# Kernel optimization log

Measured on AMD Instinct MI355X. Metric: run time of the kernel, lower is better.

## Reference

```python
import jax, jax.numpy as jnp
import numpy as np

N = 50000          # nodes
E = 500000         # edges (avg degree 10)
WIDTH = 128        # node feature width
HID = 128          # width * scale, scale=1 -> 2 heads of 64
HEAD = 64          # head_dim (module-level constant)
EMB = WIDTH // 2   # edge-embed width = 64
RES = 1.0
BOND = (5, 6, 2, 17)  # bond_size vocabularies


def setup_inputs() -> dict:
    key = jax.random.key(0)
    ks = jax.random.split(key, 24)
    w = lambda k, s: (jax.random.normal(k, s, jnp.float32) * 0.02)
    inp = {
        "x": jax.random.normal(ks[0], (N, WIDTH), jnp.float32),
        "edge_index": jax.random.randint(ks[1], (2, E), 0, N),
        "edge_attr": jax.random.randint(ks[2], (E, 4), 0, 3),
        # pre: Linear(width, width)
        "pre_w": w(ks[3], (WIDTH, WIDTH)), "pre_b": jnp.zeros((WIDTH,), jnp.float32),
        # msg[0..3]: Linear(width, hidden)
        "msg0_w": w(ks[4], (WIDTH, HID)), "msg0_b": jnp.zeros((HID,), jnp.float32),
        "msg1_w": w(ks[5], (WIDTH, HID)), "msg1_b": jnp.zeros((HID,), jnp.float32),
        "msg2_w": w(ks[6], (WIDTH, HID)), "msg2_b": jnp.zeros((HID,), jnp.float32),
        "msg3_w": w(ks[7], (WIDTH, HID)), "msg3_b": jnp.zeros((HID,), jnp.float32),
        # remix[0..2]: Linear(width//2, hidden)
        "remix0_w": w(ks[8], (EMB, HID)), "remix0_b": jnp.zeros((HID,), jnp.float32),
        "remix1_w": w(ks[9], (EMB, HID)), "remix1_b": jnp.zeros((HID,), jnp.float32),
        "remix2_w": w(ks[10], (EMB, HID)), "remix2_b": jnp.zeros((HID,), jnp.float32),
        # post: Linear(hidden, width)
        "post_w": w(ks[11], (HID, WIDTH)), "post_b": jnp.zeros((WIDTH,), jnp.float32),
        # EmbedBlock tables (bond_size + 1 rows each); tables 1..3 have padding_idx=0
        "emb0": w(ks[12], (BOND[0] + 1, EMB)),
        "emb1": w(ks[13], (BOND[1] + 1, EMB)).at[0].set(0.0),
        "emb2": w(ks[14], (BOND[2] + 1, EMB)).at[0].set(0.0),
        "emb3": w(ks[15], (BOND[3] + 1, EMB)).at[0].set(0.0),
        "einit": jnp.zeros((4,), jnp.float32),          # EmbedBlock.init0
        "init0": jnp.zeros((4,), jnp.float32),          # ConvBlock.init0 (hop*2+2)
    }
    return inp


def _gelu(v):
    return jax.nn.gelu(v, approximate=False)


def _ln(v):
    m = jnp.mean(v, axis=-1, keepdims=True)
    var = jnp.mean(jnp.square(v - m), axis=-1, keepdims=True)
    return (v - m) / jnp.sqrt(var + 1e-5)


def reference(x, edge_index, edge_attr, pre_w, pre_b, msg0_w, msg0_b,
              msg1_w, msg1_b, msg2_w, msg2_b, msg3_w, msg3_b,
              remix0_w, remix0_b, remix1_w, remix1_b, remix2_w, remix2_b,
              post_w, post_b, emb0, emb1, emb2, emb3, einit, init0):
    n = x.shape[0]
    e = edge_index.shape[1]
    xx = _ln(x @ pre_w + pre_b)  # pre: Linear + LayerNorm(no affine)
    # EmbedBlock: weighted sum of per-column embeddings, xw = exp(a)/sqrt(sum exp(a))
    xw = jnp.exp(einit) / jnp.sqrt(jnp.sum(jnp.exp(einit)))
    ee = (emb0[edge_attr[:, 0]] * xw[0] + emb1[edge_attr[:, 1]] * xw[1]
          + emb2[edge_attr[:, 2]] * xw[2] + emb3[edge_attr[:, 3]] * xw[3])  # [E, 64]
    src, dst = edge_index[0], edge_index[1]  # source_to_target: j=src, i=dst
    x_j = xx[src]
    x_i = xx[dst]
    scale_e = jnp.exp(init0[-2])
    scale_v = jnp.exp(init0[-1])
    q = x_i @ msg1_w + msg1_b + (ee @ remix0_w + remix0_b) * scale_e  # [E, HID]
    k = x_j @ msg2_w + msg2_b + (ee @ remix1_w + remix1_b) * scale_e
    v = _gelu(x_j @ msg3_w + msg3_b + (ee @ remix2_w + remix2_b) * scale_v)
    # per-head attention score, head_dim = 64
    att = jnp.sum((q * k).reshape(e, -1, HEAD), axis=-1, keepdims=True) / np.sqrt(HEAD)
    att = jnp.exp(att * init0[0] + init0[1])  # edge_type=0, hop=1
    msg = (v.reshape(e, -1, HEAD) * att).reshape(e, -1)  # [E, HID]
    agg = jax.ops.segment_sum(msg, dst, num_segments=n)  # scatter-add to targets
    xx = _gelu(xx @ msg0_w + msg0_b) + agg
    out = xx @ post_w + post_b
    return x + out * RES
```

## Files before the change

### kernel.cpp

```cpp
#include <hip/hip_runtime.h>
#include <cstdint>

#define WIDTH 128
#define NCOMBO 2268
#define XSL 136
#define OSL 132

typedef short bf16x8 __attribute__((ext_vector_type(8)));
typedef float f32x4  __attribute__((ext_vector_type(4)));

__device__ __forceinline__ float gelu_fast(float v) {
    float e = __expf(v * __builtin_fmaf(v * v, 0.0713548f, 1.5957691f));
    return v - v * __builtin_amdgcn_rcpf(e + 1.0f);
}
__device__ __forceinline__ short f2b(float f) {
    unsigned u = __float_as_uint(f);
    unsigned r = (u + 0x7FFFu + ((u >> 16) & 1u)) >> 16;
    return (short)r;
}
__device__ __forceinline__ float b2f_lo(unsigned u) { return __uint_as_float(u << 16); }
__device__ __forceinline__ float b2f_hi(unsigned u) { return __uint_as_float(u & 0xFFFF0000u); }
__device__ __forceinline__ unsigned pack2(float lo, float hi) {
    return (unsigned)(unsigned short)f2b(lo) | ((unsigned)(unsigned short)f2b(hi) << 16);
}

__global__ void k_prep(const float* __restrict__ einit, const float* __restrict__ init0,
                       const float* __restrict__ emb0, const float* __restrict__ emb1,
                       const float* __restrict__ emb2, const float* __restrict__ emb3,
                       const float* __restrict__ r0w, const float* __restrict__ r0b,
                       const float* __restrict__ r1w, const float* __restrict__ r1b,
                       const float* __restrict__ r2w, const float* __restrict__ r2b,
                       const float* __restrict__ pw0, const float* __restrict__ pw1,
                       const float* __restrict__ pw2, const float* __restrict__ pw3,
                       const float* __restrict__ pw4, const float* __restrict__ pw5,
                       short* __restrict__ o0, short* __restrict__ o1,
                       short* __restrict__ o2, short* __restrict__ o3,
                       short* __restrict__ o4, short* __restrict__ o5,
                       float* __restrict__ U, float* __restrict__ scal,
                       int* __restrict__ counts, int n) {
    int tid = blockIdx.x * blockDim.x + threadIdx.x;
    if (tid == 0) { scal[0] = init0[0]; scal[1] = init0[1]; }
    const int TOTW = 6 * 16384;
    const int TOTU = 3 * 34 * WIDTH;
    if (tid < TOTW) {
        int which = tid >> 14;
        int r = tid & 16383;
        int t    = r >> 11;
        int kc   = (r >> 9) & 3;
        int lane = (r >> 3) & 63;
        int j    = r & 7;
        int k  = kc * 32 + ((lane >> 4) << 3) + j;
        int nn = (t << 4) + (lane & 15);
        const float* w = (which == 0) ? pw0 : (which == 1) ? pw1 : (which == 2) ? pw2
                       : (which == 3) ? pw3 : (which == 4) ? pw4 : pw5;
        short* o = (which == 0) ? o0 : (which == 1) ? o1 : (which == 2) ? o2
                 : (which == 3) ? o3 : (which == 4) ? o4 : o5;
        o[r] = f2b(w[k * 128 + nn]);
    } else if (tid < TOTW + TOTU) {
        int idx = tid - TOTW;
        float e0 = expf(einit[0]), e1 = expf(einit[1]), e2 = expf(einit[2]), e3 = expf(einit[3]);
        float inv = 1.0f / sqrtf(e0 + e1 + e2 + e3);
        float xw[4] = {e0 * inv, e1 * inv, e2 * inv, e3 * inv};
        float se = expf(init0[2]);
        float sv = expf(init0[3]);
        int r   = idx / (34 * WIDTH);
        int rem = idx - r * (34 * WIDTH);
        int g   = rem / WIDTH;
        int j   = rem - g * WIDTH;
        int cc, base;
        if (g >= 16)      { cc = 3; base = 16; }
        else if (g >= 13) { cc = 2; base = 13; }
        else if (g >= 6)  { cc = 1; base = 6; }
        else              { cc = 0; base = 0; }
        int i = g - base;
        const float* em = (cc == 0) ? emb0 : (cc == 1) ? emb1 : (cc == 2) ? emb2 : emb3;
        const float* w  = (r == 0) ? r0w : (r == 1) ? r1w : r2w;
        const float* rb = (r == 0) ? r0b : (r == 1) ? r1b : r2b;
        float s = (r == 2) ? sv : se;
        float acc = 0.0f;
        const float* erow = em + i * 64;
        for (int d = 0; d < 64; ++d) acc += erow[d] * w[d * WIDTH + j];
        float val = s * xw[cc] * acc;
        if (cc == 0) val += s * rb[j];
        U[idx] = val;
    } else if (tid < TOTW + TOTU + n) {
        counts[tid - TOTW - TOTU] = 0;
    }
}

__global__ void k_prepc(const float* __restrict__ U, const float* __restrict__ init0,
                        float* __restrict__ Uc) {
    int bi = blockIdx.x;
    int r  = bi / NCOMBO;
    if (r < 2 && init0[0] == 0.0f) return;
    int cb = bi - r * NCOMBO;
    int a  = cb / 378;
    int rm = cb - a * 378;
    int b  = rm / 54;
    rm -= b * 54;
    int c  = rm / 18;
    int d  = rm - c * 18;
    int j  = threadIdx.x;
    const float* Ur = U + r * 34 * WIDTH;
    Uc[(size_t)bi * WIDTH + j] = Ur[a * WIDTH + j] + Ur[(6 + b) * WIDTH + j]
                               + Ur[(13 + c) * WIDTH + j] + Ur[(16 + d) * WIDTH + j];
}

__global__ void k_hist(const int* __restrict__ edge_index, int* __restrict__ counts,
                       int* __restrict__ rank, int E) {
    int e = blockIdx.x * blockDim.x + threadIdx.x;
    if (e >= E) return;
    rank[e] = atomicAdd(&counts[edge_index[E + e]], 1);
}

__global__ void k_scan1(const int* __restrict__ counts, int* __restrict__ lscan,
                        int* __restrict__ partials, int n) {
    __shared__ int s[256];
    int t = threadIdx.x;
    int i = blockIdx.x * 256 + t;
    int v = (i < n) ? counts[i] : 0;
    s[t] = v;
    __syncthreads();
    for (int d = 1; d < 256; d <<= 1) {
        int u = (t >= d) ? s[t - d] : 0;
        __syncthreads();
        s[t] += u;
        __syncthreads();
    }
    if (i < n) lscan[i] = s[t];
    if (t == 255) partials[blockIdx.x] = s[255];
}

__global__ void k_scan2(int* __restrict__ partials, int nb,
                        int* __restrict__ offsets, int n) {
    __shared__ int s[1024];
    int t = threadIdx.x;
    int v = (t < nb) ? partials[t] : 0;
    s[t] = v;
    __syncthreads();
    for (int d = 1; d < 1024; d <<= 1) {
        int u = (t >= d) ? s[t - d] : 0;
        __syncthreads();
        s[t] += u;
        __syncthreads();
    }
    if (t < nb) partials[t] = s[t] - v;
    if (t == 1023) offsets[n] = s[1023];
}

__global__ void k_scan3(const int* __restrict__ counts, const int* __restrict__ lscan,
                        const int* __restrict__ partials, int* __restrict__ offsets, int n) {
    int i = blockIdx.x * 256 + threadIdx.x;
    if (i >= n) return;
    offsets[i] = partials[blockIdx.x] + lscan[i] - counts[i];
}

__global__ void k_scatter(const int* __restrict__ edge_index, const int* __restrict__ edge_attr,
                          const int* __restrict__ offsets, const int* __restrict__ rank,
                          unsigned* __restrict__ s_pk, int E) {
    int e = blockIdx.x * blockDim.x + threadIdx.x;
    if (e >= E) return;
    int src = edge_index[e];
    int dst = edge_index[E + e];
    int4 at = ((const int4*)edge_attr)[e];
    int combo = ((at.x * 7 + at.y) * 3 + at.z) * 18 + at.w;
    s_pk[offsets[dst] + rank[e]] = (unsigned)src | ((unsigned)combo << 17);
}

__global__ void __launch_bounds__(256, 2) k_gemm12(
        const float* __restrict__ x,
        const short* __restrict__ preF, const float* __restrict__ pre_b,
        const short* __restrict__ w0F, const float* __restrict__ b0,
        const short* __restrict__ w1F, const float* __restrict__ b1,
        const short* __restrict__ w2F, const float* __restrict__ b2,
        const short* __restrict__ w3F, const float* __restrict__ b3,
        const float* __restrict__ scal,
        short* __restrict__ Gb, float* __restrict__ A,
        short* __restrict__ Bb, short* __restrict__ Cb, int n) {
    __shared__ short xs_raw[64 * XSL];
    __shared__ short xs_xx[64 * XSL];
    int tid  = threadIdx.x;
    int w    = tid >> 6;
    int lane = tid & 63;
    int quad = lane >> 4, l16 = lane & 15;
    int m0   = blockIdx.x * 64;

    bf16x8 Bg[2][4], Bc[2][4];
#pragma unroll
    for (int tt = 0; tt < 2; ++tt)
#pragma unroll
        for (int kc = 0; kc < 4; ++kc) {
            int fo = (((2 * w + tt) * 4 + kc) * 64 + lane) * 8;
            Bg[tt][kc] = *(const bf16x8*)(w0F + fo);
            Bc[tt][kc] = *(const bf16x8*)(w3F + fo);
        }

#pragma unroll
    for (int it = 0; it < 8; ++it) {
        int fi  = it * 256 + tid;
        int row = fi >> 5, c4 = fi & 31;
        int gr  = min(m0 + row, n - 1);
        float4 v = ((const float4*)x)[(size_t)gr * 32 + c4];
        uint2 p;
        p.x = pack2(v.x, v.y);
        p.y = pack2(v.z, v.w);
        *(uint2*)(&xs_raw[row * XSL + c4 * 4]) = p;
    }
    __syncthreads();

    {
        bf16x8 a[4];
#pragma unroll
        for (int kc = 0; kc < 4; ++kc)
            a[kc] = *(const bf16x8*)(&xs_raw[(w * 16 + l16) * XSL + kc * 32 + quad * 8]);
        f32x4 acc[8];
#pragma unroll
        for (int t = 0; t < 8; ++t) acc[t] = (f32x4){0.f, 0.f, 0.f, 0.f};
#pragma unroll
        for (int kc = 0; kc < 4; ++kc)
#pragma unroll
            for (int t = 0; t < 8; ++t) {
                bf16x8 b = *(const bf16x8*)(preF + ((t * 4 + kc) * 64 + lane) * 8);
                acc[t] = __builtin_amdgcn_mfma_f32_16x16x32_bf16(a[kc], b, acc[t], 0, 0, 0);
            }
#pragma unroll
        for (int t = 0; t < 8; ++t) {
            float bv = pre_b[t * 16 + l16];
#pragma unroll
            for (int r = 0; r < 4; ++r) acc[t][r] += bv;
        }
#pragma unroll
        for (int r = 0; r < 4; ++r) {
            float s = 0.f, s2 = 0.f;
#pragma unroll
            for (int t = 0; t < 8; ++t) { float v = acc[t][r]; s += v; s2 += v * v; }
            s  += __shfl_xor(s, 1);  s2 += __shfl_xor(s2, 1);
            s  += __shfl_xor(s, 2);  s2 += __shfl_xor(s2, 2);
            s  += __shfl_xor(s, 4);  s2 += __shfl_xor(s2, 4);
            s  += __shfl_xor(s, 8);  s2 += __shfl_xor(s2, 8);
            float m   = s * (1.0f / WIDTH);
            float var = s2 * (1.0f / WIDTH) - m * m;
            float rs  = rsqrtf(var + 1e-5f);
#pragma unroll
            for (int t = 0; t < 8; ++t) acc[t][r] = (acc[t][r] - m) * rs;
        }
        int rowb = w * 16 + quad * 4;
#pragma unroll
        for (int t = 0; t < 8; ++t)
#pragma unroll
            for (int r = 0; r < 4; ++r)
                xs_xx[(rowb + r) * XSL + t * 16 + l16] = f2b(acc[t][r]);
    }
    __syncthreads();

    bf16x8 a2[4][4];
#pragma unroll
    for (int i = 0; i < 4; ++i)
#pragma unroll
        for (int kc = 0; kc < 4; ++kc)
            a2[i][kc] = *(const bf16x8*)(&xs_xx[(i * 16 + l16) * XSL + kc * 32 + quad * 8]);
    __syncthreads();

    {
        f32x4 accG[4][2], accC[4][2];
#pragma unroll
        for (int i = 0; i < 4; ++i)
#pragma unroll
            for (int tt = 0; tt < 2; ++tt) {
                accG[i][tt] = (f32x4){0.f,0.f,0.f,0.f};
                accC[i][tt] = (f32x4){0.f,0.f,0.f,0.f};
            }
#pragma unroll
        for (int kc = 0; kc < 4; ++kc)
#pragma unroll
            for (int i = 0; i < 4; ++i)
#pragma unroll
                for (int tt = 0; tt < 2; ++tt) {
                    accG[i][tt] = __builtin_amdgcn_mfma_f32_16x16x32_bf16(a2[i][kc], Bg[tt][kc], accG[i][tt], 0, 0, 0);
                    accC[i][tt] = __builtin_amdgcn_mfma_f32_16x16x32_bf16(a2[i][kc], Bc[tt][kc], accC[i][tt], 0, 0, 0);
                }
#pragma unroll
        for (int tt = 0; tt < 2; ++tt) {
            int col = (2 * w + tt) * 16 + l16;
            float bg = b0[col];
            float bc = b3[col];
#pragma unroll
            for (int i = 0; i < 4; ++i)
#pragma unroll
                for (int r = 0; r < 4; ++r) {
                    int row = i * 16 + quad * 4 + r;
                    xs_raw[row * XSL + col] = f2b(gelu_fast(accG[i][tt][r] + bg));
                    xs_xx[row * XSL + col]  = f2b(accC[i][tt][r] + bc);
                }
        }
    }
    __syncthreads();

#pragma unroll
    for (int it = 0; it < 4; ++it) {
        int si  = it * 256 + tid;
        int row = si >> 4, c8 = si & 15;
        if (m0 + row < n) {
            *(bf16x8*)(Gb + (size_t)(m0 + row) * WIDTH + c8 * 8) = *(const bf16x8*)(&xs_raw[row * XSL + c8 * 8]);
            *(bf16x8*)(Cb + (size_t)(m0 + row) * WIDTH + c8 * 8) = *(const bf16x8*)(&xs_xx[row * XSL + c8 * 8]);
        }
    }

    if (scal[0] != 0.0f) {
        bf16x8 Ba[2][4], Bbf[2][4];
#pragma unroll
        for (int tt = 0; tt < 2; ++tt)
#pragma unroll
            for (int kc = 0; kc < 4; ++kc) {
                int fo = (((2 * w + tt) * 4 + kc) * 64 + lane) * 8;
                Ba[tt][kc]  = *(const bf16x8*)(w1F + fo);
                Bbf[tt][kc] = *(const bf16x8*)(w2F + fo);
            }
        f32x4 accA[4][2], accB[4][2];
#pragma unroll
        for (int i = 0; i < 4; ++i)
#pragma unroll
            for (int tt = 0; tt < 2; ++tt) {
                accA[i][tt] = (f32x4){0.f,0.f,0.f,0.f};
                accB[i][tt] = (f32x4){0.f,0.f,0.f,0.f};
            }
#pragma unroll
        for (int kc = 0; kc < 4; ++kc)
#pragma unroll
            for (int i = 0; i < 4; ++i)
#pragma unroll
                for (int tt = 0; tt < 2; ++tt) {
                    accA[i][tt] = __builtin_amdgcn_mfma_f32_16x16x32_bf16(a2[i][kc], Ba[tt][kc],  accA[i][tt], 0, 0, 0);
                    accB[i][tt] = __builtin_amdgcn_mfma_f32_16x16x32_bf16(a2[i][kc], Bbf[tt][kc], accB[i][tt], 0, 0, 0);
                }
#pragma unroll
        for (int tt = 0; tt < 2; ++tt) {
            int col = (2 * w + tt) * 16 + l16;
            float ba = b1[col];
            float bb = b2[col];
#pragma unroll
            for (int i = 0; i < 4; ++i)
#pragma unroll
                for (int r = 0; r < 4; ++r) {
                    int row = m0 + i * 16 + quad * 4 + r;
                    if (row < n) {
                        size_t idx = (size_t)row * WIDTH + col;
                        A[idx]  = accA[i][tt][r] + ba;
                        Bb[idx] = f2b(accB[i][tt][r] + bb);
                    }
                }
        }
    }
}

__global__ void __launch_bounds__(256)
k_agg(const int* __restrict__ offsets, const unsigned* __restrict__ s_pk,
      const float* __restrict__ A, const short* __restrict__ Bb,
      const short* __restrict__ Cb, const float* __restrict__ Uc,
      const float* __restrict__ scal, const short* __restrict__ Gb,
      short* __restrict__ hb, int n) {
    int wid = threadIdx.x >> 6;
    int L   = threadIdx.x & 63;
    int node = blockIdx.x * 4 + wid;
    if (node >= n) return;
    int start = offsets[node];
    int end   = offsets[node + 1];

    const unsigned* Cb32 = (const unsigned*)Cb;
    const unsigned* Bb32 = (const unsigned*)Bb;
    const float2* U0c2 = (const float2*)(Uc);
    const float2* U1c2 = (const float2*)(Uc + (size_t)NCOMBO * WIDTH);
    const float2* U2c2 = (const float2*)(Uc + 2 * (size_t)NCOMBO * WIDTH);

    float i0 = scal[0], i1 = scal[1];
    float acc0 = 0.0f, acc1 = 0.0f;

    if (i0 == 0.0f) {
        int p = start;
        for (; p + 4 <= end; p += 4) {
            unsigned pk0 = s_pk[p],     pk1 = s_pk[p + 1];
            unsigned pk2 = s_pk[p + 2], pk3 = s_pk[p + 3];
            unsigned cc0 = Cb32[(pk0 & 0x1FFFFu) * 64 + L];
            unsigned cc1 = Cb32[(pk1 & 0x1FFFFu) * 64 + L];
            unsigned cc2 = Cb32[(pk2 & 0x1FFFFu) * 64 + L];
            unsigned cc3 = Cb32[(pk3 & 0x1FFFFu) * 64 + L];
            float2   uu0 = U2c2[(pk0 >> 17) * 64 + L];
            float2   uu1 = U2c2[(pk1 >> 17) * 64 + L];
            float2   uu2 = U2c2[(pk2 >> 17) * 64 + L];
            float2   uu3 = U2c2[(pk3 >> 17) * 64 + L];
            acc0 += gelu_fast(b2f_lo(cc0) + uu0.x);
            acc1 += gelu_fast(b2f_hi(cc0) + uu0.y);
            acc0 += gelu_fast(b2f_lo(cc1) + uu1.x);
            acc1 += gelu_fast(b2f_hi(cc1) + uu1.y);
            acc0 += gelu_fast(b2f_lo(cc2) + uu2.x);
            acc1 += gelu_fast(b2f_hi(cc2) + uu2.y);
            acc0 += gelu_fast(b2f_lo(cc3) + uu3.x);
            acc1 += gelu_fast(b2f_hi(cc3) + uu3.y);
        }
        if (p + 2 <= end) {
            unsigned pk0 = s_pk[p], pk1 = s_pk[p + 1];
            unsigned cc0 = Cb32[(pk0 & 0x1FFFFu) * 64 + L];
            unsigned cc1 = Cb32[(pk1 & 0x1FFFFu) * 64 + L];
            float2   uu0 = U2c2[(pk0 >> 17) * 64 + L];
            float2   uu1 = U2c2[(pk1 >> 17) * 64 + L];
            acc0 += gelu_fast(b2f_lo(cc0) + uu0.x);
            acc1 += gelu_fast(b2f_hi(cc0) + uu0.y);
            acc0 += gelu_fast(b2f_lo(cc1) + uu1.x);
            acc1 += gelu_fast(b2f_hi(cc1) + uu1.y);
            p += 2;
        }
        if (p < end) {
            unsigned pk0 = s_pk[p];
            unsigned cc0 = Cb32[(pk0 & 0x1FFFFu) * 64 + L];
            float2   uu0 = U2c2[(pk0 >> 17) * 64 + L];
            acc0 += gelu_fast(b2f_lo(cc0) + uu0.x);
            acc1 += gelu_fast(b2f_hi(cc0) + uu0.y);
        }
        float s = __expf(i1);
        acc0 *= s; acc1 *= s;
    } else {
        float2 av = *(const float2*)(A + (size_t)node * WIDTH + 2 * L);
        int p = start;
        for (; p + 2 <= end; p += 2) {
            unsigned pk0 = s_pk[p], pk1 = s_pk[p + 1];
            unsigned sA = pk0 & 0x1FFFFu, cA = pk0 >> 17;
            unsigned sB = pk1 & 0x1FFFFu, cB = pk1 >> 17;
            float2 u0a = U0c2[cA * 64 + L], u0b = U0c2[cB * 64 + L];
            float2 u1a = U1c2[cA * 64 + L], u1b = U1c2[cB * 64 + L];
            float2 u2a = U2c2[cA * 64 + L], u2b = U2c2[cB * 64 + L];
            unsigned bba = Bb32[sA * 64 + L], bbb = Bb32[sB * 64 + L];
            unsigned cca = Cb32[sA * 64 + L], ccb = Cb32[sB * 64 + L];
            {
                float q0 = av.x + u0a.x, q1 = av.y + u0a.y;
                float k0 = b2f_lo(bba) + u1a.x, k1 = b2f_hi(bba) + u1a.y;
                float v0 = gelu_fast(b2f_lo(cca) + u2a.x);
                float v1 = gelu_fast(b2f_hi(cca) + u2a.y);
                float s = q0 * k0 + q1 * k1;
                s += __shfl_xor(s, 1);
                s += __shfl_xor(s, 2);
                s += __shfl_xor(s, 4);
                s += __shfl_xor(s, 8);
                s += __shfl_xor(s, 16);
                float att = __expf(s * 0.125f * i0 + i1);
                acc0 += v0 * att;
                acc1 += v1 * att;
            }
            {
                float q0 = av.x + u0b.x, q1 = av.y + u0b.y;
                float k0 = b2f_lo(bbb) + u1b.x, k1 = b2f_hi(bbb) + u1b.y;
                float v0 = gelu_fast(b2f_lo(ccb) + u2b.x);
                float v1 = gelu_fast(b2f_hi(ccb) + u2b.y);
                float s = q0 * k0 + q1 * k1;
                s += __shfl_xor(s, 1);
                s += __shfl_xor(s, 2);
                s += __shfl_xor(s, 4);
                s += __shfl_xor(s, 8);
                s += __shfl_xor(s, 16);
                float att = __expf(s * 0.125f * i0 + i1);
                acc0 += v0 * att;
                acc1 += v1 * att;
            }
        }
        if (p < end) {
            unsigned pk = s_pk[p];
            unsigned sA = pk & 0x1FFFFu, cA = pk >> 17;
            float2 u0 = U0c2[cA * 64 + L];
            float2 u1 = U1c2[cA * 64 + L];
            float2 u2 = U2c2[cA * 64 + L];
            unsigned bb = Bb32[sA * 64 + L];
            unsigned cc = Cb32[sA * 64 + L];
            float q0 = av.x + u0.x, q1 = av.y + u0.y;
            float k0 = b2f_lo(bb) + u1.x, k1 = b2f_hi(bb) + u1.y;
            float v0 = gelu_fast(b2f_lo(cc) + u2.x);
            float v1 = gelu_fast(b2f_hi(cc) + u2.y);
            float s = q0 * k0 + q1 * k1;
            s += __shfl_xor(s, 1);
            s += __shfl_xor(s, 2);
            s += __shfl_xor(s, 4);
            s += __shfl_xor(s, 8);
            s += __shfl_xor(s, 16);
            float att = __expf(s * 0.125f * i0 + i1);
            acc0 += v0 * att;
            acc1 += v1 * att;
        }
    }
    unsigned g = ((const unsigned*)Gb)[(size_t)node * 64 + L];
    ((unsigned*)hb)[(size_t)node * 64 + L] = pack2(b2f_lo(g) + acc0, b2f_hi(g) + acc1);
}

__global__ void __launch_bounds__(256, 2) k_post(
        const float* __restrict__ x, const short* __restrict__ hb,
        const short* __restrict__ postF, const float* __restrict__ post_b,
        float* __restrict__ out, int n) {
    __shared__ short hs[64 * XSL];
    __shared__ float os[64 * OSL];
    int tid  = threadIdx.x;
    int w    = tid >> 6;
    int lane = tid & 63;
    int quad = lane >> 4, l16 = lane & 15;
    int m0   = blockIdx.x * 64;

    bf16x8 Bp[2][4];
#pragma unroll
    for (int tt = 0; tt < 2; ++tt)
#pragma unroll
        for (int kc = 0; kc < 4; ++kc)
            Bp[tt][kc] = *(const bf16x8*)(postF + (((2 * w + tt) * 4 + kc) * 64 + lane) * 8);

#pragma unroll
    for (int it = 0; it < 4; ++it) {
        int si  = it * 256 + tid;
        int row = si >> 4, c8 = si & 15;
        int gr  = min(m0 + row, n - 1);
        *(bf16x8*)(&hs[row * XSL + c8 * 8]) = *(const bf16x8*)(hb + (size_t)gr * WIDTH + c8 * 8);
    }
    __syncthreads();

    bf16x8 a[4][4];
#pragma unroll
    for (int i = 0; i < 4; ++i)
#pragma unroll
        for (int kc = 0; kc < 4; ++kc)
            a[i][kc] = *(const bf16x8*)(&hs[(i * 16 + l16) * XSL + kc * 32 + quad * 8]);

    f32x4 acc[4][2];
#pragma unroll
    for (int i = 0; i < 4; ++i)
#pragma unroll
        for (int tt = 0; tt < 2; ++tt) acc[i][tt] = (f32x4){0.f,0.f,0.f,0.f};
#pragma unroll
    for (int kc = 0; kc < 4; ++kc)
#pragma unroll
        for (int i = 0; i < 4; ++i)
#pragma unroll
            for (int tt = 0; tt < 2; ++tt)
                acc[i][tt] = __builtin_amdgcn_mfma_f32_16x16x32_bf16(a[i][kc], Bp[tt][kc], acc[i][tt], 0, 0, 0);

#pragma unroll
    for (int tt = 0; tt < 2; ++tt) {
        int col = (2 * w + tt) * 16 + l16;
        float bv = post_b[col];
#pragma unroll
        for (int i = 0; i < 4; ++i)
#pragma unroll
            for (int r = 0; r < 4; ++r)
                os[(i * 16 + quad * 4 + r) * OSL + col] = acc[i][tt][r] + bv;
    }
    __syncthreads();

#pragma unroll
    for (int it = 0; it < 8; ++it) {
        int fi  = it * 256 + tid;
        int row = fi >> 5, c4 = fi & 31;
        if (m0 + row < n) {
            float4 xv = ((const float4*)x)[(size_t)(m0 + row) * 32 + c4];
            float4 av = *(const float4*)(&os[row * OSL + c4 * 4]);
            float4 ov = {xv.x + av.x, xv.y + av.y, xv.z + av.z, xv.w + av.w};
            ((float4*)out)[(size_t)(m0 + row) * 32 + c4] = ov;
        }
    }
}

extern "C" void kernel_launch(void* const* d_in, const int* in_sizes, int n_in,
                              void* d_out, int out_size, void* d_ws, size_t ws_size,
                              hipStream_t stream) {
    const float* x      = (const float*)d_in[0];
    const int*   eidx   = (const int*)d_in[1];
    const int*   eattr  = (const int*)d_in[2];
    const float* pre_w  = (const float*)d_in[3];
    const float* pre_b  = (const float*)d_in[4];
    const float* msg0_w = (const float*)d_in[5];
    const float* msg0_b = (const float*)d_in[6];
    const float* msg1_w = (const float*)d_in[7];
    const float* msg1_b = (const float*)d_in[8];
    const float* msg2_w = (const float*)d_in[9];
    const float* msg2_b = (const float*)d_in[10];
    const float* msg3_w = (const float*)d_in[11];
    const float* msg3_b = (const float*)d_in[12];
    const float* r0w    = (const float*)d_in[13];
    const float* r0b    = (const float*)d_in[14];
    const float* r1w    = (const float*)d_in[15];
    const float* r1b    = (const float*)d_in[16];
    const float* r2w    = (const float*)d_in[17];
    const float* r2b    = (const float*)d_in[18];
    const float* post_w = (const float*)d_in[19];
    const float* post_b = (const float*)d_in[20];
    const float* emb0   = (const float*)d_in[21];
    const float* emb1   = (const float*)d_in[22];
    const float* emb2   = (const float*)d_in[23];
    const float* emb3   = (const float*)d_in[24];
    const float* einit  = (const float*)d_in[25];
    const float* init0  = (const float*)d_in[26];

    int n = in_sizes[0] / WIDTH;
    int E = in_sizes[2] / 4;
    size_t NW = (size_t)n * WIDTH;

    float* ws   = (float*)d_ws;
    float* A    = ws;
    float* U    = ws + NW;
    float* Uc   = U + 3 * 34 * WIDTH;
    float* scal = Uc + 3 * (size_t)NCOMBO * WIDTH;
    short* sw   = (short*)(scal + 2);
    short* preF  = sw;
    short* w0F   = sw + 16384;
    short* w1F   = sw + 2 * 16384;
    short* w2F   = sw + 3 * 16384;
    short* w3F   = sw + 4 * 16384;
    short* postF = sw + 5 * 16384;
    short* Bb    = sw + 6 * 16384;
    short* Cb    = Bb + NW;
    short* Gb    = Cb + NW;
    short* hb    = Gb + NW;
    int*      ib       = (int*)(hb + NW);
    int*      offsets  = ib;
    int*      counts   = offsets + (n + 1);
    int*      lscan    = counts + n;
    int*      partials = lscan + n;
    int*      rank     = partials + 1024;
    unsigned* s_pk     = (unsigned*)(rank + E);

    int prep_total = 6 * 16384 + 3 * 34 * WIDTH + n;
    k_prep<<<(prep_total + 255) / 256, 256, 0, stream>>>(
        einit, init0, emb0, emb1, emb2, emb3,
        r0w, r0b, r1w, r1b, r2w, r2b,
        pre_w, msg0_w, msg1_w, msg2_w, msg3_w, post_w,
        preF, w0F, w1F, w2F, w3F, postF, U, scal, counts, n);
    k_prepc<<<3 * NCOMBO, 128, 0, stream>>>(U, init0, Uc);

    int eb = (E + 255) / 256;
    k_hist<<<eb, 256, 0, stream>>>(eidx, counts, rank, E);
    int sb = (n + 255) / 256;
    k_scan1<<<sb, 256, 0, stream>>>(counts, lscan, partials, n);
    k_scan2<<<1, 1024, 0, stream>>>(partials, sb, offsets, n);
    k_scan3<<<sb, 256, 0, stream>>>(counts, lscan, partials, offsets, n);
    k_scatter<<<eb, 256, 0, stream>>>(eidx, eattr, offsets, rank, s_pk, E);

    int gb = (n + 63) / 64;
    k_gemm12<<<gb, 256, 0, stream>>>(x, preF, pre_b, w0F, msg0_b, w1F, msg1_b,
                                     w2F, msg2_b, w3F, msg3_b, scal, Gb, A, Bb, Cb, n);
    k_agg<<<(n + 3) / 4, 256, 0, stream>>>(offsets, s_pk, A, Bb, Cb, Uc, scal, Gb, hb, n);
    k_post<<<gb, 256, 0, stream>>>(x, hb, postF, post_b, (float*)d_out, n);
}
```

Before: 240.7 us.

## Merge prep, histogram, scan and scatter stages into fewer fused launches

Cuts the launch chain from ten kernels to six. Weight conversion now shares a kernel with the edge histogram, the block scan shares one with the combo-table build, and the offset computation and CSR scatter ride as extra blocks inside the GEMM kernel. The scatter computes offsets inline from partials, lscan and counts instead of waiting on a separate scan3 pass, and counts are zeroed with a memset. This removes several launch gaps and serialisation points, but adds divergent block roles, and GEMM blocks with large LDS use may now share the GPU with light scatter blocks.

```diff
diff --git a/kernel.cpp b/kernel.cpp
--- a/kernel.cpp
+++ b/kernel.cpp
@@ -5,6 +5,8 @@
 #define NCOMBO 2268
 #define XSL 136
 #define OSL 132
+#define TOTW (6 * 16384)
+#define TOTU (3 * 34 * WIDTH)
 
 typedef short bf16x8 __attribute__((ext_vector_type(8)));
 typedef float f32x4  __attribute__((ext_vector_type(4)));
@@ -24,24 +26,23 @@
     return (unsigned)(unsigned short)f2b(lo) | ((unsigned)(unsigned short)f2b(hi) << 16);
 }
 
-__global__ void k_prep(const float* __restrict__ einit, const float* __restrict__ init0,
-                       const float* __restrict__ emb0, const float* __restrict__ emb1,
-                       const float* __restrict__ emb2, const float* __restrict__ emb3,
-                       const float* __restrict__ r0w, const float* __restrict__ r0b,
-                       const float* __restrict__ r1w, const float* __restrict__ r1b,
-                       const float* __restrict__ r2w, const float* __restrict__ r2b,
-                       const float* __restrict__ pw0, const float* __restrict__ pw1,
-                       const float* __restrict__ pw2, const float* __restrict__ pw3,
-                       const float* __restrict__ pw4, const float* __restrict__ pw5,
-                       short* __restrict__ o0, short* __restrict__ o1,
-                       short* __restrict__ o2, short* __restrict__ o3,
-                       short* __restrict__ o4, short* __restrict__ o5,
-                       float* __restrict__ U, float* __restrict__ scal,
-                       int* __restrict__ counts, int n) {
+__global__ void k_f1(const float* __restrict__ einit, const float* __restrict__ init0,
+                     const float* __restrict__ emb0, const float* __restrict__ emb1,
+                     const float* __restrict__ emb2, const float* __restrict__ emb3,
+                     const float* __restrict__ r0w, const float* __restrict__ r0b,
+                     const float* __restrict__ r1w, const float* __restrict__ r1b,
+                     const float* __restrict__ r2w, const float* __restrict__ r2b,
+                     const float* __restrict__ pw0, const float* __restrict__ pw1,
+                     const float* __restrict__ pw2, const float* __restrict__ pw3,
+                     const float* __restrict__ pw4, const float* __restrict__ pw5,
+                     short* __restrict__ o0, short* __restrict__ o1,
+                     short* __restrict__ o2, short* __restrict__ o3,
+                     short* __restrict__ o4, short* __restrict__ o5,
+                     float* __restrict__ U, float* __restrict__ scal,
+                     const int* __restrict__ edge_index, int* __restrict__ counts,
+                     int* __restrict__ rank, int E) {
     int tid = blockIdx.x * blockDim.x + threadIdx.x;
     if (tid == 0) { scal[0] = init0[0]; scal[1] = init0[1]; }
-    const int TOTW = 6 * 16384;
-    const int TOTU = 3 * 34 * WIDTH;
     if (tid < TOTW) {
         int which = tid >> 14;
         int r = tid & 16383;
@@ -83,52 +84,48 @@
         float val = s * xw[cc] * acc;
         if (cc == 0) val += s * rb[j];
         U[idx] = val;
-    } else if (tid < TOTW + TOTU + n) {
-        counts[tid - TOTW - TOTU] = 0;
-    }
-}
-
-__global__ void k_prepc(const float* __restrict__ U, const float* __restrict__ init0,
-                        float* __restrict__ Uc) {
-    int bi = blockIdx.x;
-    int r  = bi / NCOMBO;
-    if (r < 2 && init0[0] == 0.0f) return;
-    int cb = bi - r * NCOMBO;
-    int a  = cb / 378;
-    int rm = cb - a * 378;
-    int b  = rm / 54;
-    rm -= b * 54;
-    int c  = rm / 18;
-    int d  = rm - c * 18;
-    int j  = threadIdx.x;
-    const float* Ur = U + r * 34 * WIDTH;
-    Uc[(size_t)bi * WIDTH + j] = Ur[a * WIDTH + j] + Ur[(6 + b) * WIDTH + j]
-                               + Ur[(13 + c) * WIDTH + j] + Ur[(16 + d) * WIDTH + j];
-}
-
-__global__ void k_hist(const int* __restrict__ edge_index, int* __restrict__ counts,
-                       int* __restrict__ rank, int E) {
-    int e = blockIdx.x * blockDim.x + threadIdx.x;
-    if (e >= E) return;
-    rank[e] = atomicAdd(&counts[edge_index[E + e]], 1);
-}
-
-__global__ void k_scan1(const int* __restrict__ counts, int* __restrict__ lscan,
-                        int* __restrict__ partials, int n) {
-    __shared__ int s[256];
-    int t = threadIdx.x;
-    int i = blockIdx.x * 256 + t;
-    int v = (i < n) ? counts[i] : 0;
-    s[t] = v;
-    __syncthreads();
-    for (int d = 1; d < 256; d <<= 1) {
-        int u = (t >= d) ? s[t - d] : 0;
+    } else if (tid < TOTW + TOTU + E) {
+        int e = tid - TOTW - TOTU;
+        rank[e] = atomicAdd(&counts[edge_index[E + e]], 1);
+    }
+}
+
+__global__ void k_f2(const int* __restrict__ counts, int* __restrict__ lscan,
+                     int* __restrict__ partials, int n, int sb,
+                     const float* __restrict__ U, const float* __restrict__ init0,
+                     float* __restrict__ Uc) {
+    if ((int)blockIdx.x < sb) {
+        __shared__ int s[256];
+        int t = threadIdx.x;
+        int i = blockIdx.x * 256 + t;
+        int v = (i < n) ? counts[i] : 0;
+        s[t] = v;
         __syncthreads();
-        s[t] += u;
-        __syncthreads();
-    }
-    if (i < n) lscan[i] = s[t];
-    if (t == 255) partials[blockIdx.x] = s[255];
+        for (int d = 1; d < 256; d <<= 1) {
+            int u = (t >= d) ? s[t - d] : 0;
+            __syncthreads();
+            s[t] += u;
+            __syncthreads();
+        }
+        if (i < n) lscan[i] = s[t];
+        if (t == 255) partials[blockIdx.x] = s[255];
+    } else {
+        int bi = ((int)blockIdx.x - sb) * 2 + (threadIdx.x >> 7);
+        if (bi >= 3 * NCOMBO) return;
+        int r  = bi / NCOMBO;
+        if (r < 2 && init0[0] == 0.0f) return;
+        int cb = bi - r * NCOMBO;
+        int a  = cb / 378;
+        int rm = cb - a * 378;
+        int b  = rm / 54;
+        rm -= b * 54;
+        int c  = rm / 18;
+        int d  = rm - c * 18;
+        int j  = threadIdx.x & 127;
+        const float* Ur = U + r * 34 * WIDTH;
+        Uc[(size_t)bi * WIDTH + j] = Ur[a * WIDTH + j] + Ur[(6 + b) * WIDTH + j]
+                                   + Ur[(13 + c) * WIDTH + j] + Ur[(16 + d) * WIDTH + j];
+    }
 }
 
 __global__ void k_scan2(int* __restrict__ partials, int nb,
@@ -148,26 +145,7 @@
     if (t == 1023) offsets[n] = s[1023];
 }
 
-__global__ void k_scan3(const int* __restrict__ counts, const int* __restrict__ lscan,
-                        const int* __restrict__ partials, int* __restrict__ offsets, int n) {
-    int i = blockIdx.x * 256 + threadIdx.x;
-    if (i >= n) return;
-    offsets[i] = partials[blockIdx.x] + lscan[i] - counts[i];
-}
-
-__global__ void k_scatter(const int* __restrict__ edge_index, const int* __restrict__ edge_attr,
-                          const int* __restrict__ offsets, const int* __restrict__ rank,
-                          unsigned* __restrict__ s_pk, int E) {
-    int e = blockIdx.x * blockDim.x + threadIdx.x;
-    if (e >= E) return;
-    int src = edge_index[e];
-    int dst = edge_index[E + e];
-    int4 at = ((const int4*)edge_attr)[e];
-    int combo = ((at.x * 7 + at.y) * 3 + at.z) * 18 + at.w;
-    s_pk[offsets[dst] + rank[e]] = (unsigned)src | ((unsigned)combo << 17);
-}
-
-__global__ void __launch_bounds__(256, 2) k_gemm12(
+__global__ void __launch_bounds__(256, 2) k_f3(
         const float* __restrict__ x,
         const short* __restrict__ preF, const float* __restrict__ pre_b,
         const short* __restrict__ w0F, const float* __restrict__ b0,
@@ -176,10 +154,35 @@
         const short* __restrict__ w3F, const float* __restrict__ b3,
         const float* __restrict__ scal,
         short* __restrict__ Gb, float* __restrict__ A,
-        short* __restrict__ Bb, short* __restrict__ Cb, int n) {
+        short* __restrict__ Bb, short* __restrict__ Cb, int n,
+        const int* __restrict__ edge_index, const int* __restrict__ edge_attr,
+        const int* __restrict__ counts, const int* __restrict__ lscan,
+        const int* __restrict__ partials, const int* __restrict__ rank,
+        int* __restrict__ offsets, unsigned* __restrict__ s_pk, int E,
+        int gb, int eb) {
     __shared__ short xs_raw[64 * XSL];
     __shared__ short xs_xx[64 * XSL];
-    int tid  = threadIdx.x;
+    int tid = threadIdx.x;
+
+    if ((int)blockIdx.x >= gb) {
+        int rb = (int)blockIdx.x - gb;
+        if (rb < eb) {
+            int e = rb * 256 + tid;
+            if (e >= E) return;
+            int src = edge_index[e];
+            int dst = edge_index[E + e];
+            int4 at = ((const int4*)edge_attr)[e];
+            int combo = ((at.x * 7 + at.y) * 3 + at.z) * 18 + at.w;
+            int off = partials[dst >> 8] + lscan[dst] - counts[dst];
+            s_pk[off + rank[e]] = (unsigned)src | ((unsigned)combo << 17);
+        } else {
+            int i = (rb - eb) * 256 + tid;
+            if (i >= n) return;
+            offsets[i] = partials[i >> 8] + lscan[i] - counts[i];
+        }
+        return;
+    }
+
     int w    = tid >> 6;
     int lane = tid & 63;
     int quad = lane >> 4, l16 = lane & 15;
@@ -620,25 +623,29 @@
     int*      rank     = partials + 1024;
     unsigned* s_pk     = (unsigned*)(rank + E);
 
-    int prep_total = 6 * 16384 + 3 * 34 * WIDTH + n;
-    k_prep<<<(prep_total + 255) / 256, 256, 0, stream>>>(
+    hipMemsetAsync(counts, 0, (size_t)n * sizeof(int), stream);
+
+    int f1_total = TOTW + TOTU + E;
+    k_f1<<<(f1_total + 255) / 256, 256, 0, stream>>>(
         einit, init0, emb0, emb1, emb2, emb3,
         r0w, r0b, r1w, r1b, r2w, r2b,
         pre_w, msg0_w, msg1_w, msg2_w, msg3_w, post_w,
-        preF, w0F, w1F, w2F, w3F, postF, U, scal, counts, n);
-    k_prepc<<<3 * NCOMBO, 128, 0, stream>>>(U, init0, Uc);
-
+        preF, w0F, w1F, w2F, w3F, postF, U, scal,
+        eidx, counts, rank, E);
+
+    int sb  = (n + 255) / 256;
+    int pcb = (3 * NCOMBO + 1) / 2;
+    k_f2<<<sb + pcb, 256, 0, stream>>>(counts, lscan, partials, n, sb, U, init0, Uc);
+
+    k_scan2<<<1, 1024, 0, stream>>>(partials, sb, offsets, n);
+
+    int gb = (n + 63) / 64;
     int eb = (E + 255) / 256;
-    k_hist<<<eb, 256, 0, stream>>>(eidx, counts, rank, E);
-    int sb = (n + 255) / 256;
-    k_scan1<<<sb, 256, 0, stream>>>(counts, lscan, partials, n);
-    k_scan2<<<1, 1024, 0, stream>>>(partials, sb, offsets, n);
-    k_scan3<<<sb, 256, 0, stream>>>(counts, lscan, partials, offsets, n);
-    k_scatter<<<eb, 256, 0, stream>>>(eidx, eattr, offsets, rank, s_pk, E);
-
-    int gb = (n + 63) / 64;
-    k_gemm12<<<gb, 256, 0, stream>>>(x, preF, pre_b, w0F, msg0_b, w1F, msg1_b,
-                                     w2F, msg2_b, w3F, msg3_b, scal, Gb, A, Bb, Cb, n);
+    k_f3<<<gb + eb + sb, 256, 0, stream>>>(
+        x, preF, pre_b, w0F, msg0_b, w1F, msg1_b, w2F, msg2_b, w3F, msg3_b,
+        scal, Gb, A, Bb, Cb, n,
+        eidx, eattr, counts, lscan, partials, rank, offsets, s_pk, E, gb, eb);
+
     k_agg<<<(n + 3) / 4, 256, 0, stream>>>(offsets, s_pk, A, Bb, Cb, Uc, scal, Gb, hb, n);
     k_post<<<gb, 256, 0, stream>>>(x, hb, postF, post_b, (float*)d_out, n);
 }
```

New measurement: 231.3 us. -3.9%, faster.
